# Performance work log

Hardware: AMD Instinct MI355X
Metric: run time of the kernel (lower is better)

## Reference

```python
import jax, jax.numpy as jnp
import numpy as np

EPS = 1e-8  # torch F.cosine_similarity eps

B, H, K = 64, 2048, 256


def setup_inputs() -> dict:
    key = jax.random.key(0)
    k1, k2, k3, k4 = jax.random.split(key, 4)
    input_state = jax.random.normal(k1, (B, H), dtype=jnp.float32)
    knowledge_base = jax.random.normal(k2, (K, B, H), dtype=jnp.float32)
    W = jax.random.normal(k3, (H, H), dtype=jnp.float32) / np.sqrt(H)
    b = jax.random.normal(k4, (H,), dtype=jnp.float32) * 0.02
    return {"input_state": input_state, "knowledge_base": knowledge_base, "W": W, "b": b}


def reference(input_state, knowledge_base, W, b):
    # linear projection (torch Linear: x @ W.T + b)
    q = input_state @ W.T + b                      # [B, H]
    kproj = jnp.einsum('kbh,oh->kbo', knowledge_base, W) + b  # [K, B, H]
    # cosine similarity over last dim, with torch-style eps clamp on norms
    qn = jnp.maximum(jnp.linalg.norm(q, axis=-1), EPS)        # [B]
    kn = jnp.maximum(jnp.linalg.norm(kproj, axis=-1), EPS)    # [K, B]
    dots = jnp.einsum('bh,kbh->kb', q, kproj)                 # [K, B]
    scores = dots / (qn[None, :] * kn)                        # [K, B]
    # softmax over the K knowledge items
    attn = jax.nn.softmax(scores, axis=0)                     # [K, B]
    # output = input + softmax-weighted sum of (raw) knowledge items
    out = input_state + jnp.einsum('kb,kbh->bh', attn, knowledge_base)
    return out
```

## Files before the change

### kernel.cpp

```cpp
#include <hip/hip_runtime.h>
#include <hip/hip_bf16.h>

typedef unsigned short u16;
typedef unsigned int u32;
typedef unsigned long long u64;
typedef __attribute__((ext_vector_type(8))) short short8;
typedef __attribute__((ext_vector_type(4))) float float4v;

#define B_DIM 64
#define H_DIM 2048
#define K_DIM 256
#define NTHR  256

#define WS_WBF   0ull
#define WS_AQ    (8388608ull)
#define WS_Q     (WS_AQ + 524288ull)
#define WS_KN2   (WS_Q + 524288ull)
#define WS_DOTS  (WS_KN2 + 65536ull)
#define WS_KBF   (WS_DOTS + 65536ull)

__device__ __forceinline__ u16 f2bf(float f) {
    unsigned int u = __float_as_uint(f);
    unsigned int r = (u + 0x7fffu + ((u >> 16) & 1u)) >> 16;
    return (u16)r;
}

__device__ __forceinline__ u64 pack4(float4v v) {
    u64 a0 = f2bf(v.x), a1 = f2bf(v.y), a2 = f2bf(v.z), a3 = f2bf(v.w);
    return a0 | (a1 << 16) | (a2 << 32) | (a3 << 48);
}

__device__ __forceinline__ void llds16(const u16* g, u16* l) {
    __builtin_amdgcn_global_load_lds(
        (__attribute__((address_space(1))) void*)g,
        (__attribute__((address_space(3))) void*)l, 16, 0, 0);
}

__device__ __forceinline__ void gemm0_tile(const u16* __restrict__ Aq, const u16* __restrict__ Wb,
                                           float* __restrict__ qout, u16* As, u16* Bs,
                                           int nt, int ksplit) {
    const int tid = threadIdx.x;
    const int wave = tid >> 6, lane = tid & 63;
    const int l15 = lane & 15, qd = lane >> 4;
    const int wm = wave >> 1, wn = wave & 1;
    const int n0 = nt * 128;
    const int grow = lane >> 2;
    const int gcol = (((lane & 3) ^ ((lane >> 3) & 3)) * 8);
    const int sw = (l15 >> 1) & 3;
    float4v acc[4][4] = {};
    const int kb0 = ksplit * 128;
    for (int kk = 0; kk < 4; ++kk) {
        const int k0 = kb0 + kk * 32;
        #pragma unroll
        for (int i = 0; i < 2; ++i) {
            const int r = wave * 32 + i * 16;
            llds16(Wb + (size_t)(n0 + r + grow) * H_DIM + k0 + gcol, &Bs[r * 32]);
            llds16(Aq + (size_t)(r + grow) * H_DIM + k0 + gcol, &As[r * 32]);
        }
        __syncthreads();
        short8 af[4], bf_[4];
        #pragma unroll
        for (int mi = 0; mi < 4; ++mi)
            af[mi] = *(const short8*)&As[(wm * 64 + mi * 16 + l15) * 32 + ((qd ^ sw) * 8)];
        #pragma unroll
        for (int ni = 0; ni < 4; ++ni)
            bf_[ni] = *(const short8*)&Bs[(wn * 64 + ni * 16 + l15) * 32 + ((qd ^ sw) * 8)];
        #pragma unroll
        for (int mi = 0; mi < 4; ++mi)
            #pragma unroll
            for (int ni = 0; ni < 4; ++ni)
                acc[mi][ni] = __builtin_amdgcn_mfma_f32_16x16x32_bf16(af[mi], bf_[ni], acc[mi][ni], 0, 0, 0);
        __syncthreads();
    }
    const int n0w = n0 + wn * 64;
    if (wm == 0) {
        #pragma unroll
        for (int mi = 0; mi < 4; ++mi)
            #pragma unroll
            for (int reg = 0; reg < 4; ++reg) {
                const int m = mi * 16 + qd * 4 + reg;
                #pragma unroll
                for (int ni = 0; ni < 4; ++ni)
                    atomicAdd(&qout[m * H_DIM + n0w + ni * 16 + l15], acc[mi][ni][reg]);
            }
    }
}

__global__ __launch_bounds__(256) void prep_kernel(
        const float* __restrict__ W, const float* __restrict__ kb,
        const float* __restrict__ input, const float* __restrict__ bias,
        u16* __restrict__ Wb, u16* __restrict__ Kbf,
        u16* __restrict__ Aq, float* __restrict__ q,
        float* __restrict__ kn2, float* __restrict__ dots) {
    const int gid = blockIdx.x * NTHR + threadIdx.x;
    ((u64*)Wb)[gid] = pack4(((const float4v*)W)[gid]);
    {
        const float4v* s4 = (const float4v*)kb;
        u64* d8 = (u64*)Kbf;
        #pragma unroll
        for (int i = 0; i < 8; ++i)
            d8[gid + i * 1048576] = pack4(s4[gid + i * 1048576]);
    }
    if (gid < 65536) {
        u64 v = 0;
        if (gid < 32768) v = pack4(((const float4v*)input)[gid]);
        ((u64*)Aq)[gid] = v;
    }
    if (gid < 32768)
        ((float4v*)q)[gid] = ((const float4v*)bias)[gid & 511];
    if (gid < 4096) ((float4v*)kn2)[gid] = float4v{0.f, 0.f, 0.f, 0.f};
    else if (gid < 8192) ((float4v*)dots)[gid - 4096] = float4v{0.f, 0.f, 0.f, 0.f};
}

__global__ __launch_bounds__(256, 4) void mid_kernel(
        const u16* __restrict__ Aq, const u16* __restrict__ Wb, float* __restrict__ q) {
    __shared__ __align__(16) u16 As[128 * 32];
    __shared__ __align__(16) u16 Bs[128 * 32];
    gemm0_tile(Aq, Wb, q, As, Bs, blockIdx.x & 15, blockIdx.x >> 4);
}

#define TILE_BODY(T, bfC, a0C, bfN, a0N)                                        \
  {                                                                             \
    const int t_ = (T);                                                         \
    const u16* As_ = lds + (t_ & 3) * 16384;                                    \
    const u16* Bs_ = As_ + 8192;                                                \
    if (t_ + 3 < 64) stageA(t_ + 3);                                            \
    asm volatile("s_waitcnt lgkmcnt(0)" ::: "memory");                          \
    __builtin_amdgcn_sched_barrier(0);                                          \
    __builtin_amdgcn_s_setprio(1);                                              \
    _Pragma("unroll") for (int mi = 0; mi < 4; ++mi)                            \
      _Pragma("unroll") for (int ni = 0; ni < 4; ++ni)                          \
        acc[mi][ni] = __builtin_amdgcn_mfma_f32_16x16x32_bf16(a0C[mi], bfC[ni], acc[mi][ni], 0, 0, 0); \
    __builtin_amdgcn_s_setprio(0);                                              \
    __builtin_amdgcn_sched_barrier(0);                                          \
    _Pragma("unroll") for (int mi = 0; mi < 4; ++mi)                            \
        a0C[mi] = *(const short8*)&As_[aoff + (4 + mi) * 512];                  \
    if (t_ + 1 < 64) {                                                          \
      const u16* Asn_ = lds + ((t_ + 1) & 3) * 16384;                           \
      const u16* Bsn_ = Asn_ + 8192;                                            \
      _Pragma("unroll") for (int ni = 0; ni < 4; ++ni)                          \
          bfN[ni] = *(const short8*)&Bsn_[boff + ni * 512];                     \
      _Pragma("unroll") for (int mi = 0; mi < 4; ++mi)                          \
          a0N[mi] = *(const short8*)&Asn_[aoff + mi * 512];                     \
    }                                                                           \
    if (t_ + 3 < 64) stageB(t_ + 3);                                            \
    if (t_ + 1 < 64) { asm volatile("s_waitcnt lgkmcnt(8)" ::: "memory"); }     \
    else             { asm volatile("s_waitcnt lgkmcnt(0)" ::: "memory"); }     \
    __builtin_amdgcn_sched_barrier(0);                                          \
    __builtin_amdgcn_s_setprio(1);                                              \
    _Pragma("unroll") for (int mi = 0; mi < 4; ++mi)                            \
      _Pragma("unroll") for (int ni = 0; ni < 4; ++ni)                          \
        acc[4 + mi][ni] = __builtin_amdgcn_mfma_f32_16x16x32_bf16(a0C[mi], bfC[ni], acc[4 + mi][ni], 0, 0, 0); \
    __builtin_amdgcn_s_setprio(0);                                              \
    __builtin_amdgcn_sched_barrier(0);                                          \
    if (t_ <= 60) { asm volatile("s_waitcnt vmcnt(4)" ::: "memory"); }          \
    else          { asm volatile("s_waitcnt vmcnt(0)" ::: "memory"); }          \
    __builtin_amdgcn_s_barrier();                                               \
  }

__global__ __launch_bounds__(512, 2) void gemm_kernel(
        const u16* __restrict__ Kbf, const u16* __restrict__ Wb,
        const float* __restrict__ bias, const float* __restrict__ q,
        float* __restrict__ kn2, float* __restrict__ dots) {
    extern __shared__ __align__(16) u16 lds[];
    const int tid = threadIdx.x;
    const int wave = tid >> 6, lane = tid & 63;
    const int l15 = lane & 15, qd = lane >> 4;
    const int wm = wave >> 2, wn = wave & 3;
    const int nt = blockIdx.x & 7, mt = blockIdx.x >> 3;
    const int m0 = mt * 256, n0 = nt * 256;
    const int grow = wave * 16 + (lane >> 2);
    const int gcol = (((lane & 3) ^ ((lane >> 3) & 3)) * 8);
    const int sw = (l15 >> 1) & 3;

    const u16* srcA = Kbf + (size_t)(m0 + grow) * H_DIM + gcol;
    const u16* srcB = Wb + (size_t)(n0 + grow) * H_DIM + gcol;
    u16* dstBase = lds + wave * 512;

    auto stageA = [&](int t) {
        u16* d = dstBase + (t & 3) * 16384;
        const u16* s = srcA + t * 32;
        llds16(s, d);
        llds16(s + (size_t)128 * H_DIM, d + 4096);
    };
    auto stageB = [&](int t) {
        u16* d = dstBase + (t & 3) * 16384 + 8192;
        const u16* s = srcB + t * 32;
        llds16(s, d);
        llds16(s + (size_t)128 * H_DIM, d + 4096);
    };

    const int aoff = (wm * 128 + l15) * 32 + ((qd ^ sw) * 8);
    const int boff = (wn * 64 + l15) * 32 + ((qd ^ sw) * 8);

    float4v acc[8][4] = {};
    short8 bf0[4], a00[4], bf1[4], a01[4];

    stageA(0); stageB(0); stageA(1); stageB(1); stageA(2); stageB(2);
    asm volatile("s_waitcnt vmcnt(4)" ::: "memory");
    __builtin_amdgcn_sched_barrier(0);
    __builtin_amdgcn_s_barrier();
    {
        const u16* As0 = lds;
        const u16* Bs0 = lds + 8192;
        #pragma unroll
        for (int ni = 0; ni < 4; ++ni) bf0[ni] = *(const short8*)&Bs0[boff + ni * 512];
        #pragma unroll
        for (int mi = 0; mi < 4; ++mi) a00[mi] = *(const short8*)&As0[aoff + mi * 512];
    }

    for (int t = 0; t < 64; t += 2) {
        TILE_BODY(t,     bf0, a00, bf1, a01);
        TILE_BODY(t + 1, bf1, a01, bf0, a00);
    }

    const int n0w = n0 + wn * 64;
    float bv[4];
    #pragma unroll
    for (int ni = 0; ni < 4; ++ni) bv[ni] = bias[n0w + ni * 16 + l15];
    #pragma unroll
    for (int mi = 0; mi < 8; ++mi)
        #pragma unroll
        for (int reg = 0; reg < 4; ++reg) {
            const int mloc = mi * 16 + qd * 4 + reg;
            const int mg = m0 + wm * 128 + mloc;
            const float* qrow = q + (mloc & 63) * H_DIM;
            float s2 = 0.f, sd = 0.f;
            #pragma unroll
            for (int ni = 0; ni < 4; ++ni) {
                const float y = acc[mi][ni][reg] + bv[ni];
                const float qv = qrow[n0w + ni * 16 + l15];
                s2 += y * y; sd += y * qv;
            }
            #pragma unroll
            for (int off = 1; off < 16; off <<= 1) {
                s2 += __shfl_xor(s2, off);
                sd += __shfl_xor(sd, off);
            }
            if (l15 == 0) {
                atomicAdd(&kn2[mg], s2);
                atomicAdd(&dots[mg], sd);
            }
        }
}

__global__ __launch_bounds__(256) void final_kernel(
        const float* __restrict__ input, const u16* __restrict__ Kbf,
        const float* __restrict__ q, const float* __restrict__ kn2,
        const float* __restrict__ dots, float* __restrict__ out) {
    __shared__ float sm[K_DIM];
    __shared__ float buf[4];
    const int b = blockIdx.x >> 2, hc = blockIdx.x & 3, tid = threadIdx.x;
    float s = 0.f;
    #pragma unroll
    for (int i = 0; i < 8; ++i) {
        float v = q[b * H_DIM + i * 256 + tid];
        s += v * v;
    }
    #pragma unroll
    for (int o = 32; o >= 1; o >>= 1) s += __shfl_xor(s, o);
    if ((tid & 63) == 0) buf[tid >> 6] = s;
    __syncthreads();
    const float qn = fmaxf(sqrtf(buf[0] + buf[1] + buf[2] + buf[3]), 1e-8f);
    __syncthreads();
    const float kn = fmaxf(sqrtf(kn2[tid * B_DIM + b]), 1e-8f);
    const float sc = dots[tid * B_DIM + b] / (qn * kn);
    float mx = sc;
    #pragma unroll
    for (int o = 32; o >= 1; o >>= 1) mx = fmaxf(mx, __shfl_xor(mx, o));
    if ((tid & 63) == 0) buf[tid >> 6] = mx;
    __syncthreads();
    mx = fmaxf(fmaxf(buf[0], buf[1]), fmaxf(buf[2], buf[3]));
    __syncthreads();
    const float e = expf(sc - mx);
    float se = e;
    #pragma unroll
    for (int o = 32; o >= 1; o >>= 1) se += __shfl_xor(se, o);
    if ((tid & 63) == 0) buf[tid >> 6] = se;
    __syncthreads();
    se = buf[0] + buf[1] + buf[2] + buf[3];
    sm[tid] = e / se;
    __syncthreads();
    const u32* base = (const u32*)Kbf;
    const int h2 = hc * 256 + tid;
    float s0 = 0.f, s1 = 0.f;
    #pragma unroll 8
    for (int k = 0; k < K_DIM; ++k) {
        const u32 p = base[(size_t)(k * B_DIM + b) * (H_DIM / 2) + h2];
        const float a = sm[k];
        s0 += a * __uint_as_float(p << 16);
        s1 += a * __uint_as_float(p & 0xffff0000u);
    }
    const int h = h2 * 2;
    float2 iv = *(const float2*)&input[(size_t)b * H_DIM + h];
    float2 r; r.x = iv.x + s0; r.y = iv.y + s1;
    *(float2*)&out[(size_t)b * H_DIM + h] = r;
}

extern "C" void kernel_launch(void* const* d_in, const int* in_sizes, int n_in,
                              void* d_out, int out_size, void* d_ws, size_t ws_size,
                              hipStream_t stream) {
    const float* input = (const float*)d_in[0];
    const float* kb    = (const float*)d_in[1];
    const float* W     = (const float*)d_in[2];
    const float* bias  = (const float*)d_in[3];
    float* out = (float*)d_out;
    char* ws = (char*)d_ws;

    u16*   Wb   = (u16*)(ws + WS_WBF);
    u16*   Aq   = (u16*)(ws + WS_AQ);
    float* q    = (float*)(ws + WS_Q);
    float* kn2  = (float*)(ws + WS_KN2);
    float* dots = (float*)(ws + WS_DOTS);
    u16*   Kbf  = (u16*)(ws + WS_KBF);

    static int lds_set = 0;
    if (!lds_set) {
        hipFuncSetAttribute((const void*)gemm_kernel,
                            hipFuncAttributeMaxDynamicSharedMemorySize, 131072);
        lds_set = 1;
    }

    prep_kernel<<<4096, NTHR, 0, stream>>>(W, kb, input, bias, Wb, Kbf, Aq, q, kn2, dots);
    mid_kernel<<<256, NTHR, 0, stream>>>(Aq, Wb, q);
    gemm_kernel<<<512, 512, 131072, stream>>>(Kbf, Wb, bias, q, kn2, dots);
    final_kernel<<<256, NTHR, 0, stream>>>(input, Kbf, q, kn2, dots, out);
}
```

Measured before the change: 391.6 us.

## Overlap knowledge-base bf16 conversion with q GEMM and widen final reduction block

```diff
diff --git a/kernel.cpp b/kernel.cpp
--- a/kernel.cpp
+++ b/kernel.cpp
@@ -30,7 +30,7 @@
     return a0 | (a1 << 16) | (a2 << 32) | (a3 << 48);
 }
 
-__device__ __forceinline__ void llds16(const u16* g, u16* l) {
+__device__ __forceinline__ void llds16(const u16* g, const u16* l) {
     __builtin_amdgcn_global_load_lds(
         (__attribute__((address_space(1))) void*)g,
         (__attribute__((address_space(3))) void*)l, 16, 0, 0);
@@ -48,8 +48,8 @@
     const int gcol = (((lane & 3) ^ ((lane >> 3) & 3)) * 8);
     const int sw = (l15 >> 1) & 3;
     float4v acc[4][4] = {};
-    const int kb0 = ksplit * 128;
-    for (int kk = 0; kk < 4; ++kk) {
+    const int kb0 = ksplit * 512;
+    for (int kk = 0; kk < 16; ++kk) {
         const int k0 = kb0 + kk * 32;
         #pragma unroll
         for (int i = 0; i < 2; ++i) {
@@ -87,20 +87,12 @@
 }
 
 __global__ __launch_bounds__(256) void prep_kernel(
-        const float* __restrict__ W, const float* __restrict__ kb,
-        const float* __restrict__ input, const float* __restrict__ bias,
-        u16* __restrict__ Wb, u16* __restrict__ Kbf,
+        const float* __restrict__ W, const float* __restrict__ input,
+        const float* __restrict__ bias, u16* __restrict__ Wb,
         u16* __restrict__ Aq, float* __restrict__ q,
         float* __restrict__ kn2, float* __restrict__ dots) {
     const int gid = blockIdx.x * NTHR + threadIdx.x;
     ((u64*)Wb)[gid] = pack4(((const float4v*)W)[gid]);
-    {
-        const float4v* s4 = (const float4v*)kb;
-        u64* d8 = (u64*)Kbf;
-        #pragma unroll
-        for (int i = 0; i < 8; ++i)
-            d8[gid + i * 1048576] = pack4(s4[gid + i * 1048576]);
-    }
     if (gid < 65536) {
         u64 v = 0;
         if (gid < 32768) v = pack4(((const float4v*)input)[gid]);
@@ -113,17 +105,25 @@
 }
 
 __global__ __launch_bounds__(256, 4) void mid_kernel(
-        const u16* __restrict__ Aq, const u16* __restrict__ Wb, float* __restrict__ q) {
+        const float* __restrict__ kb, const u16* __restrict__ Aq,
+        const u16* __restrict__ Wb, float* __restrict__ q, u16* __restrict__ Kbf) {
     __shared__ __align__(16) u16 As[128 * 32];
     __shared__ __align__(16) u16 Bs[128 * 32];
-    gemm0_tile(Aq, Wb, q, As, Bs, blockIdx.x & 15, blockIdx.x >> 4);
+    const int bid = blockIdx.x;
+    if (bid < 64) {
+        gemm0_tile(Aq, Wb, q, As, Bs, bid & 15, bid >> 4);
+    } else {
+        const float4v* s4 = (const float4v*)kb;
+        u64* d8 = (u64*)Kbf;
+        for (int i = (bid - 64) * NTHR + threadIdx.x; i < 8388608; i += 960 * NTHR)
+            d8[i] = pack4(s4[i]);
+    }
 }
 
 #define TILE_BODY(T, bfC, a0C, bfN, a0N)                                        \
   {                                                                             \
     const int t_ = (T);                                                         \
     const u16* As_ = lds + (t_ & 3) * 16384;                                    \
-    const u16* Bs_ = As_ + 8192;                                                \
     if (t_ + 3 < 64) stageA(t_ + 3);                                            \
     asm volatile("s_waitcnt lgkmcnt(0)" ::: "memory");                          \
     __builtin_amdgcn_sched_barrier(0);                                          \
@@ -244,57 +244,76 @@
         }
 }
 
-__global__ __launch_bounds__(256) void final_kernel(
+__global__ __launch_bounds__(1024) void final_kernel(
         const float* __restrict__ input, const u16* __restrict__ Kbf,
         const float* __restrict__ q, const float* __restrict__ kn2,
         const float* __restrict__ dots, float* __restrict__ out) {
     __shared__ float sm[K_DIM];
-    __shared__ float buf[4];
+    __shared__ float buf[24];
+    __shared__ float2 part[1024];
     const int b = blockIdx.x >> 2, hc = blockIdx.x & 3, tid = threadIdx.x;
+    const int wave = tid >> 6, lane = tid & 63;
     float s = 0.f;
     #pragma unroll
-    for (int i = 0; i < 8; ++i) {
-        float v = q[b * H_DIM + i * 256 + tid];
+    for (int i = 0; i < 2; ++i) {
+        float v = q[b * H_DIM + i * 1024 + tid];
         s += v * v;
     }
     #pragma unroll
     for (int o = 32; o >= 1; o >>= 1) s += __shfl_xor(s, o);
-    if ((tid & 63) == 0) buf[tid >> 6] = s;
-    __syncthreads();
-    const float qn = fmaxf(sqrtf(buf[0] + buf[1] + buf[2] + buf[3]), 1e-8f);
-    __syncthreads();
-    const float kn = fmaxf(sqrtf(kn2[tid * B_DIM + b]), 1e-8f);
-    const float sc = dots[tid * B_DIM + b] / (qn * kn);
-    float mx = sc;
-    #pragma unroll
-    for (int o = 32; o >= 1; o >>= 1) mx = fmaxf(mx, __shfl_xor(mx, o));
-    if ((tid & 63) == 0) buf[tid >> 6] = mx;
-    __syncthreads();
-    mx = fmaxf(fmaxf(buf[0], buf[1]), fmaxf(buf[2], buf[3]));
-    __syncthreads();
-    const float e = expf(sc - mx);
-    float se = e;
-    #pragma unroll
-    for (int o = 32; o >= 1; o >>= 1) se += __shfl_xor(se, o);
-    if ((tid & 63) == 0) buf[tid >> 6] = se;
-    __syncthreads();
-    se = buf[0] + buf[1] + buf[2] + buf[3];
-    sm[tid] = e / se;
-    __syncthreads();
-    const u32* base = (const u32*)Kbf;
-    const int h2 = hc * 256 + tid;
+    if (lane == 0) buf[wave] = s;
+    __syncthreads();
+    float qs = 0.f;
+    #pragma unroll
+    for (int i = 0; i < 16; ++i) qs += buf[i];
+    const float qn = fmaxf(sqrtf(qs), 1e-8f);
+    __syncthreads();
+    float sc = 0.f;
+    if (tid < K_DIM) {
+        const float kn = fmaxf(sqrtf(kn2[tid * B_DIM + b]), 1e-8f);
+        sc = dots[tid * B_DIM + b] / (qn * kn);
+        float mx = sc;
+        #pragma unroll
+        for (int o = 32; o >= 1; o >>= 1) mx = fmaxf(mx, __shfl_xor(mx, o));
+        if (lane == 0) buf[16 + wave] = mx;
+    }
+    __syncthreads();
+    const float mx = fmaxf(fmaxf(buf[16], buf[17]), fmaxf(buf[18], buf[19]));
+    __syncthreads();
+    if (tid < K_DIM) {
+        const float e = expf(sc - mx);
+        float se = e;
+        #pragma unroll
+        for (int o = 32; o >= 1; o >>= 1) se += __shfl_xor(se, o);
+        if (lane == 0) buf[20 + wave] = se;
+        sm[tid] = e;
+    }
+    __syncthreads();
+    const float sei = 1.f / (buf[20] + buf[21] + buf[22] + buf[23]);
+    __syncthreads();
+    const int col = tid & 255, quarter = tid >> 8;
+    const int h2 = hc * 256 + col;
+    const u32* basep = (const u32*)Kbf + ((size_t)(quarter * 64 * B_DIM + b)) * (H_DIM / 2) + h2;
+    const float* smq = sm + quarter * 64;
     float s0 = 0.f, s1 = 0.f;
     #pragma unroll 8
-    for (int k = 0; k < K_DIM; ++k) {
-        const u32 p = base[(size_t)(k * B_DIM + b) * (H_DIM / 2) + h2];
-        const float a = sm[k];
+    for (int i = 0; i < 64; ++i) {
+        const u32 p = basep[(size_t)i * (B_DIM * H_DIM / 2)];
+        const float a = smq[i];
         s0 += a * __uint_as_float(p << 16);
         s1 += a * __uint_as_float(p & 0xffff0000u);
     }
-    const int h = h2 * 2;
-    float2 iv = *(const float2*)&input[(size_t)b * H_DIM + h];
-    float2 r; r.x = iv.x + s0; r.y = iv.y + s1;
-    *(float2*)&out[(size_t)b * H_DIM + h] = r;
+    part[tid] = float2{s0, s1};
+    __syncthreads();
+    if (tid < 256) {
+        float2 p0 = part[tid], p1 = part[256 + tid], p2 = part[512 + tid], p3 = part[768 + tid];
+        const int h = h2 * 2;
+        float2 iv = *(const float2*)&input[(size_t)b * H_DIM + h];
+        float2 r;
+        r.x = iv.x + (p0.x + p1.x + p2.x + p3.x) * sei;
+        r.y = iv.y + (p0.y + p1.y + p2.y + p3.y) * sei;
+        *(float2*)&out[(size_t)b * H_DIM + h] = r;
+    }
 }
 
 extern "C" void kernel_launch(void* const* d_in, const int* in_sizes, int n_in,
@@ -321,8 +340,8 @@
         lds_set = 1;
     }
 
-    prep_kernel<<<4096, NTHR, 0, stream>>>(W, kb, input, bias, Wb, Kbf, Aq, q, kn2, dots);
-    mid_kernel<<<256, NTHR, 0, stream>>>(Aq, Wb, q);
+    prep_kernel<<<4096, NTHR, 0, stream>>>(W, input, bias, Wb, Aq, q, kn2, dots);
+    mid_kernel<<<1024, NTHR, 0, stream>>>(kb, Aq, Wb, q, Kbf);
     gemm_kernel<<<512, 512, 131072, stream>>>(Kbf, Wb, bias, q, kn2, dots);
-    final_kernel<<<256, NTHR, 0, stream>>>(input, Kbf, q, kn2, dots, out);
-}
+    final_kernel<<<256, 1024, 0, stream>>>(input, Kbf, q, kn2, dots, out);
+}
```

Measured after the change: 367.1 us. -6.3%, faster.
